# Kernel tuning notes

Measured on AMD Instinct MI355X. Metric: run time of the kernel, lower is better.

The kernel has to match this reference:

```python
import jax, jax.numpy as jnp
import numpy as np

D = 1024
H = 16
DH = D // H
NEG = -10000000.0


def setup_inputs() -> dict:
    key = jax.random.key(0)
    ks = jax.random.split(key, 12)
    B, L = 2, 2048
    sc = 0.02
    inp = {
        "q": jax.random.normal(ks[0], (B, L, D), jnp.float32),
        "k": jax.random.normal(ks[1], (B, L, D), jnp.float32),
        "v": jax.random.normal(ks[2], (B, L, D), jnp.float32),
        "attention_mask": jax.random.randint(ks[3], (B, L, L), 0, 2) == 1,
        "head_mask": jnp.ones((1, 1, 1), jnp.float32),
        "Wq": sc * jax.random.normal(ks[4], (D, D), jnp.float32),
        "bq": jnp.zeros((D,), jnp.float32),
        "Wk": sc * jax.random.normal(ks[5], (D, D), jnp.float32),
        "bk": jnp.zeros((D,), jnp.float32),
        "Wv": sc * jax.random.normal(ks[6], (D, D), jnp.float32),
        "bv": jnp.zeros((D,), jnp.float32),
        "Wo": sc * jax.random.normal(ks[7], (D, D), jnp.float32),
        "bo": jnp.zeros((D,), jnp.float32),
    }
    return inp


def reference(q, k, v, attention_mask, head_mask, Wq, bq, Wk, bk, Wv, bv, Wo, bo):
    B, Lq, _ = q.shape
    Lk = k.shape[1]
    # QKV projections (nn.Linear: x @ W.T + b), split into heads
    qh = (q @ Wq.T + bq).reshape(B, Lq, H, DH)  # [B,Lq,H,dh]
    kh = (k @ Wk.T + bk).reshape(B, Lk, H, DH)
    vh = (v @ Wv.T + bv).reshape(B, Lk, H, DH)
    # scores [B,H,Lq,Lk], scaled by 1/sqrt(dh)
    scores = jnp.einsum("bihd,bjhd->bhij", qh, kh) / jnp.sqrt(jnp.float32(DH))
    scores = jnp.where(attention_mask[:, None, :, :], NEG, scores)
    probs = jax.nn.softmax(scores, axis=-1)
    probs = probs * head_mask  # broadcastable head mask (dropout is identity in eval)
    ctx = jnp.einsum("bhij,bjhd->bihd", probs, vh).reshape(B, Lq, D)
    # output linear + residual (Add_and_LN with with_lN=False, eval dropout)
    out = ctx @ Wo.T + bo + q
    return out
```

## Files before the change

### kernel.cpp

```cpp
#include <hip/hip_runtime.h>

typedef unsigned short u16;
typedef unsigned long long u64;
typedef __attribute__((ext_vector_type(4))) float f32x4;
typedef __attribute__((ext_vector_type(8))) short s16x8;
typedef __attribute__((ext_vector_type(4))) short s16x4;
typedef __attribute__((ext_vector_type(4))) unsigned int u32x4;

#define LDS_LOAD16(gp, lp) __builtin_amdgcn_global_load_lds( \
    (__attribute__((address_space(1))) void*)(gp), \
    (__attribute__((address_space(3))) void*)(lp), 16, 0, 0)

#define MFMA16 __builtin_amdgcn_mfma_f32_16x16x32_bf16

constexpr float L2E = 1.44269504088896340736f;

__device__ __forceinline__ u16 f2bf(float x) {
  unsigned u = __float_as_uint(x);
  u += 0x7FFF + ((u >> 16) & 1);
  return (u16)(u >> 16);
}

__device__ __forceinline__ unsigned cvtpk_bf16(float lo, float hi) {
  unsigned r;
  asm("v_cvt_pk_bf16_f32 %0, %1, %2" : "=v"(r) : "v"(lo), "v"(hi));
  return r;
}

struct ConvArgs {
  const float* src[7];
  u16* dst[7];
  int n4[7];
  float scale[7];
};

__global__ __launch_bounds__(256) void convert_many(ConvArgs a) {
  const int arr = blockIdx.y;
  const f32x4* src = (const f32x4*)a.src[arr];
  u16* dst = a.dst[arr];
  const int n4 = a.n4[arr];
  const float sc = a.scale[arr];
  const int stride = gridDim.x * blockDim.x;
  for (int i = blockIdx.x * blockDim.x + threadIdx.x; i < n4; i += stride) {
    f32x4 v = src[i];
    s16x4 o;
#pragma unroll
    for (int j = 0; j < 4; ++j) o[j] = (short)f2bf(v[j] * sc);
    *(s16x4*)(dst + (size_t)i * 4) = o;
  }
}

__global__ __launch_bounds__(256) void mask_to_bits(const unsigned int* __restrict__ m32,
                                                    u64* __restrict__ bits,
                                                    int n) {
  const int lane = threadIdx.x & 63;
  unsigned probe = m32[lane];
  bool bytemode = __any(probe > 1u);
  const int stride = gridDim.x * blockDim.x;
  for (int i = blockIdx.x * blockDim.x + threadIdx.x; i < n; i += stride) {
    bool v;
    if (bytemode) v = ((const unsigned char*)m32)[i] != 0;
    else          v = m32[i] != 0;
    u64 b = __ballot(v);
    if (lane == 0) bits[i >> 6] = b;
  }
}

struct QkvArgsB {
  const u16* A[3];
  const u16* B[3];
  const float* bias[3];
  float bscale[3];
  u16* C[3];
};

__global__ __launch_bounds__(256) void gemm_qkv_bf(QkvArgsB a) {
  const int z = blockIdx.z;
  const u16* __restrict__ A = a.A[z];
  const u16* __restrict__ B = a.B[z];
  const float* __restrict__ bias = a.bias[z];
  const float bscale = a.bscale[z];
  u16* __restrict__ C = a.C[z];

  __shared__ u16 As[3][4096];
  __shared__ u16 Bs[3][4096];
  const int tid = threadIdx.x;
  const int lane = tid & 63;
  const int wave = tid >> 6;
  const int g = lane >> 4, c = lane & 15;
  const int g4 = g * 4;
  const int bx = blockIdx.x;
  const int row0 = (((bx & 7) << 2) | (bx >> 3)) * 128;
  const int col0 = blockIdx.y * 128;
  const int wr = (wave >> 1) * 64, wc = (wave & 1) * 64;

  f32x4 acc[4][4] = {};

#define STAGE_QKV(p_, k0_) { _Pragma("unroll") \
    for (int i = 0; i < 2; ++i) { \
      int e = (i * 256 + tid) * 8; \
      LDS_LOAD16(A + (size_t)(row0 + (e >> 5)) * 1024 + (k0_) + (e & 31), As[p_] + e); \
      LDS_LOAD16(B + (size_t)(col0 + (e >> 5)) * 1024 + (k0_) + (e & 31), Bs[p_] + e); } }

  STAGE_QKV(0, 0);
  STAGE_QKV(1, 32);

  for (int s = 0; s < 32; ++s) {
    const int p = s % 3;
    if (s == 31) asm volatile("s_waitcnt vmcnt(0)" ::: "memory");
    else         asm volatile("s_waitcnt vmcnt(4)" ::: "memory");
    __builtin_amdgcn_s_barrier();
    __builtin_amdgcn_sched_barrier(0);
    if (s + 2 < 32) {
      const int np = (s + 2) % 3;
      STAGE_QKV(np, (s + 2) * 32);
    }
    s16x8 af[4], bf[4];
#pragma unroll
    for (int m = 0; m < 4; ++m) af[m] = *(const s16x8*)(As[p] + (wr + m * 16 + c) * 32 + g * 8);
#pragma unroll
    for (int n = 0; n < 4; ++n) bf[n] = *(const s16x8*)(Bs[p] + (wc + n * 16 + c) * 32 + g * 8);
#pragma unroll
    for (int m = 0; m < 4; ++m)
#pragma unroll
      for (int n = 0; n < 4; ++n)
        acc[m][n] = MFMA16(bf[n], af[m], acc[m][n], 0, 0, 0);
  }

  f32x4 bv[4];
#pragma unroll
  for (int n = 0; n < 4; ++n) {
    bv[n] = *(const f32x4*)(bias + col0 + wc + n * 16 + g4);
#pragma unroll
    for (int r = 0; r < 4; ++r) bv[n][r] *= bscale;
  }
#pragma unroll
  for (int m = 0; m < 4; ++m)
#pragma unroll
    for (int n = 0; n < 4; ++n) {
      s16x4 o;
#pragma unroll
      for (int r = 0; r < 4; ++r) o[r] = (short)f2bf(acc[m][n][r] + bv[n][r]);
      *(s16x4*)(C + (size_t)(row0 + wr + m * 16 + c) * 1024 + col0 + wc + n * 16 + g4) = o;
    }
}

struct QkvArgsF {
  const float* A[3];
  const u16* B[3];
  const float* bias[3];
  float bscale[3];
  u16* C[3];
};

__global__ __launch_bounds__(256) void gemm_qkv_f32(QkvArgsF a) {
  const int z = blockIdx.z;
  const float* __restrict__ A = a.A[z];
  const u16* __restrict__ B = a.B[z];
  const float* __restrict__ bias = a.bias[z];
  const float bscale = a.bscale[z];
  u16* __restrict__ C = a.C[z];

  __shared__ u16 As[2][4096];
  __shared__ u16 Bs[2][4096];
  const int tid = threadIdx.x;
  const int lane = tid & 63;
  const int wave = tid >> 6;
  const int g = lane >> 4, c = lane & 15;
  const int g4 = g * 4;
  const int row0 = blockIdx.x * 128;
  const int col0 = blockIdx.y * 128;
  const int wr = (wave >> 1) * 64, wc = (wave & 1) * 64;
  const int ra = tid >> 2;
  const int cca = (tid & 3) * 8;

  f32x4 acc[4][4] = {};
  f32x4 ar[2][2];
#pragma unroll
  for (int i = 0; i < 2; ++i) {
    ar[i][0] = *(const f32x4*)(A + (size_t)(row0 + i * 64 + ra) * 1024 + cca);
    ar[i][1] = *(const f32x4*)(A + (size_t)(row0 + i * 64 + ra) * 1024 + cca + 4);
  }

  for (int s = 0; s < 32; ++s) {
    const int p = s & 1;
    const int k0 = s * 32;
#pragma unroll
    for (int i = 0; i < 2; ++i) {
      unsigned w0 = cvtpk_bf16(ar[i][0][0], ar[i][0][1]);
      unsigned w1 = cvtpk_bf16(ar[i][0][2], ar[i][0][3]);
      unsigned w2 = cvtpk_bf16(ar[i][1][0], ar[i][1][1]);
      unsigned w3 = cvtpk_bf16(ar[i][1][2], ar[i][1][3]);
      union { u32x4 u; s16x8 v; } w;
      w.u = (u32x4){w0, w1, w2, w3};
      *(s16x8*)(As[p] + (i * 256 + tid) * 8) = w.v;
    }
    if (s < 31) {
#pragma unroll
      for (int i = 0; i < 2; ++i) {
        ar[i][0] = *(const f32x4*)(A + (size_t)(row0 + i * 64 + ra) * 1024 + k0 + 32 + cca);
        ar[i][1] = *(const f32x4*)(A + (size_t)(row0 + i * 64 + ra) * 1024 + k0 + 32 + cca + 4);
      }
    }
#pragma unroll
    for (int i = 0; i < 2; ++i) {
      int e = (i * 256 + tid) * 8;
      LDS_LOAD16(B + (size_t)(col0 + (e >> 5)) * 1024 + k0 + (e & 31), Bs[p] + e);
    }
    __syncthreads();

    s16x8 af[4], bf[4];
#pragma unroll
    for (int m = 0; m < 4; ++m) af[m] = *(const s16x8*)(As[p] + (wr + m * 16 + c) * 32 + g * 8);
#pragma unroll
    for (int n = 0; n < 4; ++n) bf[n] = *(const s16x8*)(Bs[p] + (wc + n * 16 + c) * 32 + g * 8);
#pragma unroll
    for (int m = 0; m < 4; ++m)
#pragma unroll
      for (int n = 0; n < 4; ++n)
        acc[m][n] = MFMA16(bf[n], af[m], acc[m][n], 0, 0, 0);
  }

  f32x4 bv[4];
#pragma unroll
  for (int n = 0; n < 4; ++n) {
    bv[n] = *(const f32x4*)(bias + col0 + wc + n * 16 + g4);
#pragma unroll
    for (int r = 0; r < 4; ++r) bv[n][r] *= bscale;
  }
#pragma unroll
  for (int m = 0; m < 4; ++m)
#pragma unroll
    for (int n = 0; n < 4; ++n) {
      s16x4 o;
#pragma unroll
      for (int r = 0; r < 4; ++r) o[r] = (short)f2bf(acc[m][n][r] + bv[n][r]);
      *(s16x4*)(C + (size_t)(row0 + wr + m * 16 + c) * 1024 + col0 + wc + n * 16 + g4) = o;
    }
}

__global__ __launch_bounds__(256) void gemm_out(const u16* __restrict__ A,
                                                const u16* __restrict__ B,
                                                const float* __restrict__ bias,
                                                const float* __restrict__ resid,
                                                float* __restrict__ C) {
  __shared__ u16 As[3][2048];
  __shared__ u16 Bs[3][4096];
  const int tid = threadIdx.x;
  const int lane = tid & 63;
  const int wave = tid >> 6;
  const int g = lane >> 4, c = lane & 15;
  const int g4 = g * 4;
  const int bx = blockIdx.x;
  const int row0 = (((bx & 7) << 3) | (bx >> 3)) * 64;
  const int col0 = blockIdx.y * 128;
  const int wr = (wave >> 1) * 32, wc = (wave & 1) * 64;

  f32x4 acc[2][4] = {};

#define STAGE_OUT(p_, k0_) { \
    LDS_LOAD16(A + (size_t)(row0 + (tid >> 2)) * 1024 + (k0_) + (tid & 3) * 8, As[p_] + tid * 8); \
    _Pragma("unroll") \
    for (int i = 0; i < 2; ++i) { \
      int e = (i * 256 + tid) * 8; \
      LDS_LOAD16(B + (size_t)(col0 + (e >> 5)) * 1024 + (k0_) + (e & 31), Bs[p_] + e); } }

  STAGE_OUT(0, 0);
  STAGE_OUT(1, 32);

  for (int s = 0; s < 32; ++s) {
    const int p = s % 3;
    if (s == 31) asm volatile("s_waitcnt vmcnt(0)" ::: "memory");
    else         asm volatile("s_waitcnt vmcnt(3)" ::: "memory");
    __builtin_amdgcn_s_barrier();
    __builtin_amdgcn_sched_barrier(0);
    if (s + 2 < 32) {
      const int np = (s + 2) % 3;
      STAGE_OUT(np, (s + 2) * 32);
    }
    s16x8 af[2], bf[4];
#pragma unroll
    for (int m = 0; m < 2; ++m) af[m] = *(const s16x8*)(As[p] + (wr + m * 16 + c) * 32 + g * 8);
#pragma unroll
    for (int n = 0; n < 4; ++n) bf[n] = *(const s16x8*)(Bs[p] + (wc + n * 16 + c) * 32 + g * 8);
#pragma unroll
    for (int m = 0; m < 2; ++m)
#pragma unroll
      for (int n = 0; n < 4; ++n)
        acc[m][n] = MFMA16(bf[n], af[m], acc[m][n], 0, 0, 0);
  }

  f32x4 bv[4];
#pragma unroll
  for (int n = 0; n < 4; ++n) bv[n] = *(const f32x4*)(bias + col0 + wc + n * 16 + g4);
#pragma unroll
  for (int m = 0; m < 2; ++m)
#pragma unroll
    for (int n = 0; n < 4; ++n) {
      size_t off = (size_t)(row0 + wr + m * 16 + c) * 1024 + col0 + wc + n * 16 + g4;
      f32x4 rv = *(const f32x4*)(resid + off);
      f32x4 o;
#pragma unroll
      for (int r = 0; r < 4; ++r) o[r] = acc[m][n][r] + bv[n][r] + rv[r];
      *(f32x4*)(C + off) = o;
    }
}

constexpr float NEGV = -10000000.0f;

__global__ __launch_bounds__(256) void attn_kernel(const u16* __restrict__ Qh,
                                                   const u16* __restrict__ Kh,
                                                   const u16* __restrict__ Vh,
                                                   const u64* __restrict__ mbits,
                                                   const float* __restrict__ head_mask,
                                                   u16* __restrict__ ctx) {
  __shared__ u16 Ks[2][4096];
  __shared__ u16 Vt[2][64 * 72];

  const int tid = threadIdx.x;
  const int lane = tid & 63;
  const int wave = tid >> 6;
  const int g = lane >> 4, c = lane & 15;
  const int g4 = g * 4;
  const int wid = (blockIdx.x & 7) * 64 + (blockIdx.x >> 3);
  const int qt = wid & 15;
  const int bh = wid >> 4;
  const int b = bh >> 4;
  const int h = bh & 15;
  const size_t rowbase = (size_t)b * 2048;
  const int D = 1024;

  s16x8 qf[2][2];
#pragma unroll
  for (int s = 0; s < 2; ++s) {
    const int qrow = qt * 128 + s * 64 + wave * 16 + c;
#pragma unroll
    for (int ks = 0; ks < 2; ++ks)
      qf[s][ks] = *(const s16x8*)(Qh + (rowbase + qrow) * D + h * 64 + ks * 32 + g * 8);
  }

  f32x4 accO[2][4] = {};
  f32x4 accSum[2] = {};

  union { u32x4 u; s16x8 v; } onesu;
  onesu.u = (u32x4){0x3F803F80u, 0x3F803F80u, 0x3F803F80u, 0x3F803F80u};
  const s16x8 onesA = onesu.v;

  const u64* mrow0 = mbits + (rowbase + qt * 128 + 0 * 64 + wave * 16 + c) * 32;
  const u64* mrow1 = mbits + (rowbase + qt * 128 + 1 * 64 + wave * 16 + c) * 32;

  const int kkK = tid & 63;
  const int aV = tid >> 3;
  const int sV = tid & 7;
  const int dcV = sV * 8;
  const int k2 = 2 * aV;
  const int slotV = (k2 & 32) | (((k2 >> 2) & 3) << 3) | (((k2 >> 4) & 1) << 2) | (k2 & 3);
  const int colV = slotV ^ (8 * sV);

  const u16* Kbase = Kh + rowbase * D + h * 64;
  const u16* Vbase = Vh + rowbase * D + h * 64;

  s16x8 kreg[2], vreg[2];
#define LOADKV(kb_) { \
    kreg[0] = *(const s16x8*)(Kbase + (size_t)((kb_) + kkK) * D + wave * 8); \
    kreg[1] = *(const s16x8*)(Kbase + (size_t)((kb_) + kkK) * D + (4 + wave) * 8); \
    vreg[0] = *(const s16x8*)(Vbase + (size_t)((kb_) + k2) * D + dcV); \
    vreg[1] = *(const s16x8*)(Vbase + (size_t)((kb_) + k2 + 1) * D + dcV); }
#define WRITEKV(p_) { \
    *(s16x8*)(Ks[p_] + tid * 8) = kreg[0]; \
    *(s16x8*)(Ks[p_] + 2048 + tid * 8) = kreg[1]; \
    const unsigned* v0w = (const unsigned*)&vreg[0]; \
    const unsigned* v1w = (const unsigned*)&vreg[1]; \
    _Pragma("unroll") \
    for (int j = 0; j < 8; ++j) { \
      unsigned pk = __builtin_amdgcn_perm(v1w[j >> 1], v0w[j >> 1], \
                                          (j & 1) ? 0x07060302u : 0x05040100u); \
      *(unsigned*)(Vt[p_] + (dcV + j) * 72 + colV) = pk; } }

  LOADKV(0);
  WRITEKV(0);
  LOADKV(64);
  __syncthreads();

#define ATTN_ITER(p_, it_) { \
    const int it = (it_); \
    if (it < 31) WRITEKV(p_ ^ 1); \
    if (it < 30) LOADKV((it + 2) * 64); \
    f32x4 accS[2][4]; \
    _Pragma("unroll") \
    for (int t = 0; t < 4; ++t) { \
      s16x8 kf0 = *(const s16x8*)(Ks[p_] + ((0 + g) * 64 + t * 16 + c) * 8); \
      s16x8 kf1 = *(const s16x8*)(Ks[p_] + ((4 + g) * 64 + t * 16 + c) * 8); \
      f32x4 z0 = {0.f, 0.f, 0.f, 0.f}; \
      z0 = MFMA16(kf0, qf[0][0], z0, 0, 0, 0); \
      accS[0][t] = MFMA16(kf1, qf[0][1], z0, 0, 0, 0); \
      f32x4 z1 = {0.f, 0.f, 0.f, 0.f}; \
      z1 = MFMA16(kf0, qf[1][0], z1, 0, 0, 0); \
      accS[1][t] = MFMA16(kf1, qf[1][1], z1, 0, 0, 0); \
    } \
    s16x8 vbr[4][2]; \
    _Pragma("unroll") \
    for (int d0 = 0; d0 < 4; ++d0) { \
      const int dd = d0 * 16 + c; \
      const int sw8 = (d0 * 2 + (c >> 3)) * 8; \
      _Pragma("unroll") \
      for (int ks = 0; ks < 2; ++ks) \
        vbr[d0][ks] = *(const s16x8*)(Vt[p_] + dd * 72 + ((ks * 32 + g * 8) ^ sw8)); \
    } \
    s16x8 pa[2][2]; \
    _Pragma("unroll") \
    for (int s = 0; s < 2; ++s) { \
      u64 mw = (s == 0 ? mrow0 : mrow1)[it]; \
      u64 sh = mw >> g4; \
      unsigned mlo = (unsigned)sh, mhi = (unsigned)(sh >> 32); \
      unsigned pk0[4], pk1[4]; \
      _Pragma("unroll") \
      for (int t = 0; t < 4; ++t) { \
        unsigned msrc = (t < 2) ? mlo : mhi; \
        _Pragma("unroll") \
        for (int r = 0; r < 4; ++r) { \
          float sv = accS[s][t][r]; \
          if ((msrc >> ((t & 1) * 16 + r)) & 1) sv = NEGV; \
          float pv; \
          asm("v_exp_f32 %0, %1" : "=v"(pv) : "v"(sv)); \
          accS[s][t][r] = pv; \
        } \
        pk0[t] = cvtpk_bf16(accS[s][t][0], accS[s][t][1]); \
        pk1[t] = cvtpk_bf16(accS[s][t][2], accS[s][t][3]); \
      } \
      _Pragma("unroll") \
      for (int ks = 0; ks < 2; ++ks) { \
        union { u32x4 u; s16x8 v; } w; \
        w.u = (u32x4){pk0[2 * ks], pk1[2 * ks], pk0[2 * ks + 1], pk1[2 * ks + 1]}; \
        pa[s][ks] = w.v; \
      } \
    } \
    _Pragma("unroll") \
    for (int d0 = 0; d0 < 4; ++d0) \
      _Pragma("unroll") \
      for (int ks = 0; ks < 2; ++ks) { \
        accO[0][d0] = MFMA16(vbr[d0][ks], pa[0][ks], accO[0][d0], 0, 0, 0); \
        accO[1][d0] = MFMA16(vbr[d0][ks], pa[1][ks], accO[1][d0], 0, 0, 0); \
      } \
    _Pragma("unroll") \
    for (int ks = 0; ks < 2; ++ks) { \
      accSum[0] = MFMA16(onesA, pa[0][ks], accSum[0], 0, 0, 0); \
      accSum[1] = MFMA16(onesA, pa[1][ks], accSum[1], 0, 0, 0); \
    } \
    asm volatile("s_waitcnt lgkmcnt(0)" ::: "memory"); \
    __builtin_amdgcn_s_barrier(); \
    __builtin_amdgcn_sched_barrier(0); }

  for (int it2 = 0; it2 < 16; ++it2) {
    ATTN_ITER(0, 2 * it2);
    ATTN_ITER(1, 2 * it2 + 1);
  }

  const float hm = head_mask[0];
#pragma unroll
  for (int s = 0; s < 2; ++s) {
    float inv = hm / accSum[s][0];
    const int qrow = qt * 128 + s * 64 + wave * 16 + c;
#pragma unroll
    for (int d0 = 0; d0 < 4; ++d0) {
      s16x4 o;
#pragma unroll
      for (int r = 0; r < 4; ++r) o[r] = (short)f2bf(accO[s][d0][r] * inv);
      *(s16x4*)(ctx + (rowbase + qrow) * D + h * 64 + d0 * 16 + g4) = o;
    }
  }
}

extern "C" void kernel_launch(void* const* d_in, const int* in_sizes, int n_in,
                              void* d_out, int out_size, void* d_ws, size_t ws_size,
                              hipStream_t stream) {
  const float* q  = (const float*)d_in[0];
  const float* k  = (const float*)d_in[1];
  const float* v  = (const float*)d_in[2];
  const void*  am = d_in[3];
  const float* hm = (const float*)d_in[4];
  const float* Wq = (const float*)d_in[5];
  const float* bq = (const float*)d_in[6];
  const float* Wk = (const float*)d_in[7];
  const float* bk = (const float*)d_in[8];
  const float* Wv = (const float*)d_in[9];
  const float* bv = (const float*)d_in[10];
  const float* Wo = (const float*)d_in[11];
  const float* bo = (const float*)d_in[12];

  char* ws = (char*)d_ws;
  const size_t MB = 1024 * 1024;
  const bool big = ws_size >= 58 * MB;

  if (big) {
    u16* qb  = (u16*)(ws + 0 * MB);
    u16* kb  = (u16*)(ws + 8 * MB);
    u16* vb  = (u16*)(ws + 16 * MB);
    u16* wqb = (u16*)(ws + 24 * MB);
    u16* wkb = (u16*)(ws + 26 * MB);
    u16* wvb = (u16*)(ws + 28 * MB);
    u16* wob = (u16*)(ws + 30 * MB);
    u16* Qh  = (u16*)(ws + 32 * MB);
    u16* Kh  = (u16*)(ws + 40 * MB);
    u16* Vh  = (u16*)(ws + 48 * MB);
    u64* mbits = (u64*)(ws + 56 * MB);
    u16* ctx = qb;

    ConvArgs ca;
    ca.src[0] = q;  ca.dst[0] = qb;  ca.n4[0] = 1048576; ca.scale[0] = 1.f;
    ca.src[1] = k;  ca.dst[1] = kb;  ca.n4[1] = 1048576; ca.scale[1] = 1.f;
    ca.src[2] = v;  ca.dst[2] = vb;  ca.n4[2] = 1048576; ca.scale[2] = 1.f;
    ca.src[3] = Wq; ca.dst[3] = wqb; ca.n4[3] = 262144;  ca.scale[3] = 0.125f * L2E;
    ca.src[4] = Wk; ca.dst[4] = wkb; ca.n4[4] = 262144;  ca.scale[4] = 1.f;
    ca.src[5] = Wv; ca.dst[5] = wvb; ca.n4[5] = 262144;  ca.scale[5] = 1.f;
    ca.src[6] = Wo; ca.dst[6] = wob; ca.n4[6] = 262144;  ca.scale[6] = 1.f;
    convert_many<<<dim3(512, 7), 256, 0, stream>>>(ca);

    mask_to_bits<<<2048, 256, 0, stream>>>((const unsigned int*)am, mbits, 8388608);

    QkvArgsB ga;
    ga.A[0] = qb; ga.B[0] = wqb; ga.bias[0] = bq; ga.bscale[0] = 0.125f * L2E; ga.C[0] = Qh;
    ga.A[1] = kb; ga.B[1] = wkb; ga.bias[1] = bk; ga.bscale[1] = 1.f;          ga.C[1] = Kh;
    ga.A[2] = vb; ga.B[2] = wvb; ga.bias[2] = bv; ga.bscale[2] = 1.f;          ga.C[2] = Vh;
    gemm_qkv_bf<<<dim3(32, 8, 3), 256, 0, stream>>>(ga);

    attn_kernel<<<512, 256, 0, stream>>>(Qh, Kh, Vh, mbits, hm, ctx);

    gemm_out<<<dim3(64, 8), 256, 0, stream>>>(ctx, wob, bo, q, (float*)d_out);
  } else {
    u16* Qh  = (u16*)(ws + 0 * MB);
    u16* Kh  = (u16*)(ws + 8 * MB);
    u16* Vh  = (u16*)(ws + 16 * MB);
    u16* wqb = (u16*)(ws + 24 * MB);
    u16* wkb = (u16*)(ws + 26 * MB);
    u16* wvb = (u16*)(ws + 28 * MB);
    u16* wob = (u16*)(ws + 30 * MB);
    u64* mbits = (u64*)(ws + 32 * MB);
    u16* ctx = (u16*)(ws + 33 * MB);

    ConvArgs ca;
    ca.src[0] = Wq; ca.dst[0] = wqb; ca.n4[0] = 262144; ca.scale[0] = 0.125f * L2E;
    ca.src[1] = Wk; ca.dst[1] = wkb; ca.n4[1] = 262144; ca.scale[1] = 1.f;
    ca.src[2] = Wv; ca.dst[2] = wvb; ca.n4[2] = 262144; ca.scale[2] = 1.f;
    ca.src[3] = Wo; ca.dst[3] = wob; ca.n4[3] = 262144; ca.scale[3] = 1.f;
    convert_many<<<dim3(256, 4), 256, 0, stream>>>(ca);

    mask_to_bits<<<2048, 256, 0, stream>>>((const unsigned int*)am, mbits, 8388608);

    QkvArgsF ga;
    ga.A[0] = q; ga.B[0] = wqb; ga.bias[0] = bq; ga.bscale[0] = 0.125f * L2E; ga.C[0] = Qh;
    ga.A[1] = k; ga.B[1] = wkb; ga.bias[1] = bk; ga.bscale[1] = 1.f;          ga.C[1] = Kh;
    ga.A[2] = v; ga.B[2] = wvb; ga.bias[2] = bv; ga.bscale[2] = 1.f;          ga.C[2] = Vh;
    gemm_qkv_f32<<<dim3(32, 8, 3), 256, 0, stream>>>(ga);

    attn_kernel<<<512, 256, 0, stream>>>(Qh, Kh, Vh, mbits, hm, ctx);

    gemm_out<<<dim3(64, 8), 256, 0, stream>>>(ctx, wob, bo, q, (float*)d_out);
  }
}
```

Measured before the change: 146.6 us.

## Process two 64-key tiles per barrier and prefetch mask words into registers

The attention loop now stages 128 keys per pipeline step, holding two K/V halves in double-buffered LDS, so there is one barrier and one global prefetch round per 128 keys instead of per 64. The mask bit words for the next step are loaded ahead into registers, so they are not fetched inside the softmax. This halves the number of synchronisation points and gives more compute per step to hide memory latency. In exchange it doubles the LDS footprint and the prefetch register count, which may lower occupancy.

```diff
diff --git a/kernel.cpp b/kernel.cpp
--- a/kernel.cpp
+++ b/kernel.cpp
@@ -314,8 +314,8 @@
                                                    const u64* __restrict__ mbits,
                                                    const float* __restrict__ head_mask,
                                                    u16* __restrict__ ctx) {
-  __shared__ u16 Ks[2][4096];
-  __shared__ u16 Vt[2][64 * 72];
+  __shared__ u16 Ks[2][2][4096];
+  __shared__ u16 Vt[2][2][64 * 72];
 
   const int tid = threadIdx.x;
   const int lane = tid & 63;
@@ -360,37 +360,46 @@
   const u16* Kbase = Kh + rowbase * D + h * 64;
   const u16* Vbase = Vh + rowbase * D + h * 64;
 
-  s16x8 kreg[2], vreg[2];
-#define LOADKV(kb_) { \
-    kreg[0] = *(const s16x8*)(Kbase + (size_t)((kb_) + kkK) * D + wave * 8); \
-    kreg[1] = *(const s16x8*)(Kbase + (size_t)((kb_) + kkK) * D + (4 + wave) * 8); \
-    vreg[0] = *(const s16x8*)(Vbase + (size_t)((kb_) + k2) * D + dcV); \
-    vreg[1] = *(const s16x8*)(Vbase + (size_t)((kb_) + k2 + 1) * D + dcV); }
-#define WRITEKV(p_) { \
-    *(s16x8*)(Ks[p_] + tid * 8) = kreg[0]; \
-    *(s16x8*)(Ks[p_] + 2048 + tid * 8) = kreg[1]; \
-    const unsigned* v0w = (const unsigned*)&vreg[0]; \
-    const unsigned* v1w = (const unsigned*)&vreg[1]; \
+  s16x8 kregA[2], kregB[2], vregA[2], vregB[2];
+#define LOADKV2(kb_) { \
+    kregA[0] = *(const s16x8*)(Kbase + (size_t)((kb_) + kkK) * D + wave * 8); \
+    kregA[1] = *(const s16x8*)(Kbase + (size_t)((kb_) + kkK) * D + (4 + wave) * 8); \
+    kregB[0] = *(const s16x8*)(Kbase + (size_t)((kb_) + 64 + kkK) * D + wave * 8); \
+    kregB[1] = *(const s16x8*)(Kbase + (size_t)((kb_) + 64 + kkK) * D + (4 + wave) * 8); \
+    vregA[0] = *(const s16x8*)(Vbase + (size_t)((kb_) + k2) * D + dcV); \
+    vregA[1] = *(const s16x8*)(Vbase + (size_t)((kb_) + k2 + 1) * D + dcV); \
+    vregB[0] = *(const s16x8*)(Vbase + (size_t)((kb_) + 64 + k2) * D + dcV); \
+    vregB[1] = *(const s16x8*)(Vbase + (size_t)((kb_) + 64 + k2 + 1) * D + dcV); }
+#define WRITEV1(p_, h_, vr_) { \
+    const unsigned* v0w = (const unsigned*)&vr_[0]; \
+    const unsigned* v1w = (const unsigned*)&vr_[1]; \
     _Pragma("unroll") \
     for (int j = 0; j < 8; ++j) { \
       unsigned pk = __builtin_amdgcn_perm(v1w[j >> 1], v0w[j >> 1], \
                                           (j & 1) ? 0x07060302u : 0x05040100u); \
-      *(unsigned*)(Vt[p_] + (dcV + j) * 72 + colV) = pk; } }
-
-  LOADKV(0);
-  WRITEKV(0);
-  LOADKV(64);
+      *(unsigned*)(Vt[p_][h_] + (dcV + j) * 72 + colV) = pk; } }
+#define WRITEKV2(p_) { \
+    *(s16x8*)(Ks[p_][0] + tid * 8) = kregA[0]; \
+    *(s16x8*)(Ks[p_][0] + 2048 + tid * 8) = kregA[1]; \
+    *(s16x8*)(Ks[p_][1] + tid * 8) = kregB[0]; \
+    *(s16x8*)(Ks[p_][1] + 2048 + tid * 8) = kregB[1]; \
+    WRITEV1(p_, 0, vregA); \
+    WRITEV1(p_, 1, vregB); }
+
+  LOADKV2(0);
+  WRITEKV2(0);
+  LOADKV2(128);
   __syncthreads();
 
-#define ATTN_ITER(p_, it_) { \
-    const int it = (it_); \
-    if (it < 31) WRITEKV(p_ ^ 1); \
-    if (it < 30) LOADKV((it + 2) * 64); \
+  u64 mA0 = mrow0[0], mA1 = mrow1[0];
+  u64 mB0 = mrow0[1], mB1 = mrow1[1];
+
+#define ATTN_HALF(p_, h_, mw0_, mw1_) { \
     f32x4 accS[2][4]; \
     _Pragma("unroll") \
     for (int t = 0; t < 4; ++t) { \
-      s16x8 kf0 = *(const s16x8*)(Ks[p_] + ((0 + g) * 64 + t * 16 + c) * 8); \
-      s16x8 kf1 = *(const s16x8*)(Ks[p_] + ((4 + g) * 64 + t * 16 + c) * 8); \
+      s16x8 kf0 = *(const s16x8*)(Ks[p_][h_] + ((0 + g) * 64 + t * 16 + c) * 8); \
+      s16x8 kf1 = *(const s16x8*)(Ks[p_][h_] + ((4 + g) * 64 + t * 16 + c) * 8); \
       f32x4 z0 = {0.f, 0.f, 0.f, 0.f}; \
       z0 = MFMA16(kf0, qf[0][0], z0, 0, 0, 0); \
       accS[0][t] = MFMA16(kf1, qf[0][1], z0, 0, 0, 0); \
@@ -405,12 +414,12 @@
       const int sw8 = (d0 * 2 + (c >> 3)) * 8; \
       _Pragma("unroll") \
       for (int ks = 0; ks < 2; ++ks) \
-        vbr[d0][ks] = *(const s16x8*)(Vt[p_] + dd * 72 + ((ks * 32 + g * 8) ^ sw8)); \
+        vbr[d0][ks] = *(const s16x8*)(Vt[p_][h_] + dd * 72 + ((ks * 32 + g * 8) ^ sw8)); \
     } \
     s16x8 pa[2][2]; \
     _Pragma("unroll") \
     for (int s = 0; s < 2; ++s) { \
-      u64 mw = (s == 0 ? mrow0 : mrow1)[it]; \
+      u64 mw = (s == 0) ? (mw0_) : (mw1_); \
       u64 sh = mw >> g4; \
       unsigned mlo = (unsigned)sh, mhi = (unsigned)(sh >> 32); \
       unsigned pk0[4], pk1[4]; \
@@ -446,14 +455,25 @@
     for (int ks = 0; ks < 2; ++ks) { \
       accSum[0] = MFMA16(onesA, pa[0][ks], accSum[0], 0, 0, 0); \
       accSum[1] = MFMA16(onesA, pa[1][ks], accSum[1], 0, 0, 0); \
-    } \
+    } }
+
+#define ATTN_SUPER(p_, I_) { \
+    const int I = (I_); \
+    if (I < 15) WRITEKV2(p_ ^ 1); \
+    if (I < 14) LOADKV2((I + 2) * 128); \
+    u64 nA0 = 0, nA1 = 0, nB0 = 0, nB1 = 0; \
+    if (I < 15) { nA0 = mrow0[2 * I + 2]; nA1 = mrow1[2 * I + 2]; \
+                  nB0 = mrow0[2 * I + 3]; nB1 = mrow1[2 * I + 3]; } \
+    ATTN_HALF(p_, 0, mA0, mA1); \
+    ATTN_HALF(p_, 1, mB0, mB1); \
+    mA0 = nA0; mA1 = nA1; mB0 = nB0; mB1 = nB1; \
     asm volatile("s_waitcnt lgkmcnt(0)" ::: "memory"); \
     __builtin_amdgcn_s_barrier(); \
     __builtin_amdgcn_sched_barrier(0); }
 
-  for (int it2 = 0; it2 < 16; ++it2) {
-    ATTN_ITER(0, 2 * it2);
-    ATTN_ITER(1, 2 * it2 + 1);
+  for (int I2 = 0; I2 < 8; ++I2) {
+    ATTN_SUPER(0, 2 * I2);
+    ATTN_SUPER(1, 2 * I2 + 1);
   }
 
   const float hm = head_mask[0];
```

Result: slower. 151.6 us (+3.5%).
